# Kernel tuning notes

Hardware: AMD Instinct MI355X
Metric: run time of the kernel (lower is better)

The kernel has to match this reference:

```python
import jax, jax.numpy as jnp
import numpy as np

B, S, D, H = 4, 2048, 1024, 16
DK = D // H


def setup_inputs() -> dict:
    key = jax.random.key(0)
    ks = jax.random.split(key, 11)
    inp = {
        'query': jax.random.normal(ks[0], (B, S, D), jnp.float32),
        'key': jax.random.normal(ks[1], (B, S, D), jnp.float32),
        'value': jax.random.normal(ks[2], (B, S, D), jnp.float32),
        'mask': jnp.tril(jnp.ones((1, 1, S, S), dtype=bool)),  # causal
    }
    sc = 1.0 / np.sqrt(D)
    inp['w_q'] = jax.random.normal(ks[3], (D, D), jnp.float32) * sc
    inp['b_q'] = jnp.zeros((D,), jnp.float32)
    inp['w_k'] = jax.random.normal(ks[4], (D, D), jnp.float32) * sc
    inp['b_k'] = jnp.zeros((D,), jnp.float32)
    inp['w_v'] = jax.random.normal(ks[5], (D, D), jnp.float32) * sc
    inp['b_v'] = jnp.zeros((D,), jnp.float32)
    inp['w_o'] = jax.random.normal(ks[6], (D, D), jnp.float32) * sc
    inp['b_o'] = jnp.zeros((D,), jnp.float32)
    return inp


def _split_heads(x):
    # Faithful to source: view(B, S, d_k, H) then permute(0,3,1,2)
    b, s, _ = x.shape
    return x.reshape(b, s, DK, H).transpose(0, 3, 1, 2)  # (B, H, S, DK)


def _concat_heads(x):
    # permute(0,2,1,3) -> reshape(B, S, d_k*H)
    b, h, s, dk = x.shape
    return x.transpose(0, 2, 1, 3).reshape(b, s, dk * h)


def reference(query, key, value, mask, w_q, b_q, w_k, b_k, w_v, b_v, w_o, b_o):
    q = query @ w_q.T + b_q
    k = key @ w_k.T + b_k
    v = value @ w_v.T + b_v
    q, k, v = _split_heads(q), _split_heads(k), _split_heads(v)
    scale = 1.0 / jnp.sqrt(jnp.asarray(DK, q.dtype))
    scores = jnp.einsum('bhqd,bhkd->bhqk', q, k) * scale
    scores = jnp.where(mask, scores, -jnp.inf)
    attn = jax.nn.softmax(scores, axis=-1)  # dropout p=0 -> identity
    out = jnp.einsum('bhqk,bhkd->bhqd', attn, v)
    return _concat_heads(out) @ w_o.T + b_o
```

## Files before the change

### kernel.cpp

```cpp
#include <hip/hip_runtime.h>

#define BB 4
#define SS 2048
#define DD 1024
#define HH 16
#define DK 64
#define MM (BB * SS)

typedef __bf16 bf16x8 __attribute__((ext_vector_type(8)));
typedef float f32x4 __attribute__((ext_vector_type(4)));
typedef unsigned short us8 __attribute__((ext_vector_type(8)));
typedef unsigned short us4 __attribute__((ext_vector_type(4)));

#define MFMA_BF16(a, b, c) __builtin_amdgcn_mfma_f32_16x16x32_bf16((a), (b), (c), 0, 0, 0)

__device__ __forceinline__ unsigned short f2bf(float f) {
  return __builtin_bit_cast(unsigned short, (__bf16)f);
}

__device__ __forceinline__ bf16x8 ld_frag(const unsigned short* p) {
  return __builtin_bit_cast(bf16x8, *(const us8*)p);
}

__device__ __forceinline__ void gl_lds16(const unsigned short* g, unsigned short* l) {
  __builtin_amdgcn_global_load_lds((const __attribute__((address_space(1))) void*)g,
                                   (__attribute__((address_space(3))) void*)l, 16, 0, 0);
}

__global__ void cvt_weights(const float* __restrict__ w0, const float* __restrict__ w1,
                            const float* __restrict__ w2, const float* __restrict__ w3,
                            unsigned short* __restrict__ dst) {
  const float* src = (blockIdx.y == 0) ? w0 : (blockIdx.y == 1) ? w1 : (blockIdx.y == 2) ? w2 : w3;
  unsigned short* d = dst + (size_t)blockIdx.y * (DD * DD);
  int idx = (blockIdx.x * 256 + threadIdx.x) * 4;
  float4 v = *(const float4*)(src + idx);
  us4 o;
  o[0] = f2bf(v.x); o[1] = f2bf(v.y); o[2] = f2bf(v.z); o[3] = f2bf(v.w);
  *(us4*)(d + idx) = o;
}

__global__ __launch_bounds__(256, 4) void qkv_gemm(
    const float* __restrict__ xq, const float* __restrict__ xk, const float* __restrict__ xv,
    const unsigned short* __restrict__ wb,
    const float* __restrict__ bq, const float* __restrict__ bk, const float* __restrict__ bv,
    unsigned short* __restrict__ qh, unsigned short* __restrict__ kh,
    unsigned short* __restrict__ vt) {
  const int mode = blockIdx.z;
  const float* x = (mode == 0) ? xq : (mode == 1) ? xk : xv;
  const unsigned short* w = wb + (size_t)mode * (DD * DD);
  const float* bias = (mode == 0) ? bq : (mode == 1) ? bk : bv;

  const int m0 = blockIdx.x * 128;
  const int h0 = blockIdx.y * 2;

  __shared__ unsigned short smem[17408];
  unsigned short* sA = smem;
  unsigned short* sB = smem + 8192;

  const int tid = threadIdx.x;
  const int lane = tid & 63;
  const int wave = tid >> 6;
  const int wm = wave & 1, wn = wave >> 1;
  const int quad = lane >> 4, l16 = lane & 15;

  f32x4 acc[4][4];
#pragma unroll
  for (int i = 0; i < 4; i++)
#pragma unroll
    for (int j = 0; j < 4; j++) acc[i][j] = f32x4{0.f, 0.f, 0.f, 0.f};

  const int arow = tid >> 1, ahalf = tid & 1;
  const float* ag = x + (size_t)(m0 + arow) * DD + ahalf * 32;
  unsigned short* adst = sA + ahalf * 4096 + arow * 32;

  for (int k0 = 0; k0 < DD; k0 += 64) {
    __syncthreads();
#pragma unroll
    for (int j = 0; j < 4; j++) {
      int cid = tid + j * 256;
      int half = cid >> 9;
      int rr = (cid & 511) >> 2;
      int c8 = (cid & 3) << 3;
      int n = ((rr & 63) << 4) + h0 + (rr >> 6);
      gl_lds16(w + (size_t)n * DD + k0 + half * 32 + c8,
               sB + half * 4096 + rr * 32 + c8);
    }
    {
      const float* a = ag + k0;
      float4 v0 = *(const float4*)(a + 0);
      float4 v1 = *(const float4*)(a + 4);
      float4 v2 = *(const float4*)(a + 8);
      float4 v3 = *(const float4*)(a + 12);
      float4 v4 = *(const float4*)(a + 16);
      float4 v5 = *(const float4*)(a + 20);
      float4 v6 = *(const float4*)(a + 24);
      float4 v7 = *(const float4*)(a + 28);
      us8 o0, o1, o2, o3;
      o0[0] = f2bf(v0.x); o0[1] = f2bf(v0.y); o0[2] = f2bf(v0.z); o0[3] = f2bf(v0.w);
      o0[4] = f2bf(v1.x); o0[5] = f2bf(v1.y); o0[6] = f2bf(v1.z); o0[7] = f2bf(v1.w);
      o1[0] = f2bf(v2.x); o1[1] = f2bf(v2.y); o1[2] = f2bf(v2.z); o1[3] = f2bf(v2.w);
      o1[4] = f2bf(v3.x); o1[5] = f2bf(v3.y); o1[6] = f2bf(v3.z); o1[7] = f2bf(v3.w);
      o2[0] = f2bf(v4.x); o2[1] = f2bf(v4.y); o2[2] = f2bf(v4.z); o2[3] = f2bf(v4.w);
      o2[4] = f2bf(v5.x); o2[5] = f2bf(v5.y); o2[6] = f2bf(v5.z); o2[7] = f2bf(v5.w);
      o3[0] = f2bf(v6.x); o3[1] = f2bf(v6.y); o3[2] = f2bf(v6.z); o3[3] = f2bf(v6.w);
      o3[4] = f2bf(v7.x); o3[5] = f2bf(v7.y); o3[6] = f2bf(v7.z); o3[7] = f2bf(v7.w);
      *(us8*)(adst + 0) = o0;
      *(us8*)(adst + 8) = o1;
      *(us8*)(adst + 16) = o2;
      *(us8*)(adst + 24) = o3;
    }
    __syncthreads();
#pragma unroll
    for (int kk = 0; kk < 2; kk++) {
      bf16x8 af[4];
#pragma unroll
      for (int mi = 0; mi < 4; mi++)
        af[mi] = ld_frag(sA + kk * 4096 + (wm * 64 + mi * 16 + l16) * 32 + quad * 8);
#pragma unroll
      for (int ni = 0; ni < 4; ni++) {
        bf16x8 bfr = ld_frag(sB + kk * 4096 + (wn * 64 + ni * 16 + l16) * 32 + quad * 8);
#pragma unroll
        for (int mi = 0; mi < 4; mi++) acc[mi][ni] = MFMA_BF16(af[mi], bfr, acc[mi][ni]);
      }
    }
  }

  if (mode < 2) {
    unsigned short* outp = (mode == 0) ? qh : kh;
#pragma unroll
    for (int mi = 0; mi < 4; mi++) {
#pragma unroll
      for (int ni = 0; ni < 4; ni++) {
        int c = wn * 64 + ni * 16 + l16;
        int h = h0 + (c >> 6), dk = c & 63;
        float bvv = bias[(dk << 4) + h];
        int mg0 = m0 + wm * 64 + mi * 16 + quad * 4;
#pragma unroll
        for (int r = 0; r < 4; r++) {
          int mg = mg0 + r;
          int bb = mg >> 11, s = mg & 2047;
          size_t dst = ((size_t)((bb << 4) + h) * SS + s) * DK + dk;
          outp[dst] = f2bf(acc[mi][ni][r] + bvv);
        }
      }
    }
  } else {
    __syncthreads();
#pragma unroll
    for (int mi = 0; mi < 4; mi++) {
#pragma unroll
      for (int ni = 0; ni < 4; ni++) {
        int c = wn * 64 + ni * 16 + l16;
        int h = h0 + (c >> 6), dk = c & 63;
        float bvv = bias[(dk << 4) + h];
        int ml0 = wm * 64 + mi * 16 + quad * 4;
#pragma unroll
        for (int r = 0; r < 4; r++)
          smem[c * 136 + ml0 + r] = f2bf(acc[mi][ni][r] + bvv);
      }
    }
    __syncthreads();
    int bb = m0 >> 11;
    int sbase = m0 & 2047;
#pragma unroll
    for (int i = 0; i < 8; i++) {
      int idx = tid + i * 256;
      int c = idx >> 4, mc = (idx & 15) << 3;
      int h = h0 + (c >> 6), dk = c & 63;
      size_t dst = ((size_t)((bb << 4) + h) * DK + dk) * SS + sbase + mc;
      *(us8*)(vt + dst) = *(const us8*)(smem + c * 136 + mc);
    }
  }
}

__global__ __launch_bounds__(256, 2) void attn(
    const unsigned short* __restrict__ qh, const unsigned short* __restrict__ kh,
    const unsigned short* __restrict__ vt, unsigned short* __restrict__ outc) {
  const int bh = blockIdx.x;
  const int by = blockIdx.y;
  const int b = bh >> 4, h = bh & 15;
  const unsigned short* Qp = qh + (size_t)bh * SS * DK;
  const unsigned short* Kp = kh + (size_t)bh * SS * DK;
  const unsigned short* Vp = vt + (size_t)bh * DK * SS;

  __shared__ unsigned short sK[128 * 72];
  __shared__ unsigned short sV[64 * 136];

  const int tid = threadIdx.x;
  const int lane = tid & 63;
  const int wave = tid >> 6;
  const int quad = lane >> 4, l16 = lane & 15;
  const int wq0 = wave * 32;

  const float sl = 0.125f * 1.44269504088896f;

  for (int pass = 0; pass < 2; pass++) {
    const int qt = pass ? (15 - by) : by;
    const int q0 = qt * 128;

    bf16x8 aq[2][2];
#pragma unroll
    for (int mi = 0; mi < 2; mi++)
#pragma unroll
      for (int kk = 0; kk < 2; kk++)
        aq[mi][kk] = ld_frag(Qp + (size_t)(q0 + wq0 + mi * 16 + l16) * DK + kk * 32 + quad * 8);

    f32x4 o_acc[2][4];
    float mrowL[2], lrowL[2];
#pragma unroll
    for (int mi = 0; mi < 2; mi++) {
#pragma unroll
      for (int ni = 0; ni < 4; ni++) o_acc[mi][ni] = f32x4{0.f, 0.f, 0.f, 0.f};
      mrowL[mi] = -1e30f;
      lrowL[mi] = 0.f;
    }

    for (int kt = 0; kt <= qt; kt++) {
      const int k0 = kt * 128;
      const bool diag = (kt == qt);
      __syncthreads();
#pragma unroll
      for (int i = 0; i < 4; i++) {
        int idx = tid + i * 256;
        int row = idx >> 3, c8 = (idx & 7) << 3;
        *(us8*)(sK + row * 72 + c8) = *(const us8*)(Kp + (size_t)(k0 + row) * DK + c8);
      }
#pragma unroll
      for (int i = 0; i < 4; i++) {
        int idx = tid + i * 256;
        int row = idx >> 4, cc = (idx & 15) << 3;
        *(us8*)(sV + row * 136 + cc) = *(const us8*)(Vp + (size_t)row * SS + k0 + cc);
      }
      __syncthreads();

      f32x4 sc[2][8];
#pragma unroll
      for (int mi = 0; mi < 2; mi++)
#pragma unroll
        for (int kti = 0; kti < 8; kti++) sc[mi][kti] = f32x4{0.f, 0.f, 0.f, 0.f};
#pragma unroll
      for (int kti = 0; kti < 8; kti++) {
#pragma unroll
        for (int kk = 0; kk < 2; kk++) {
          bf16x8 ak = ld_frag(sK + (kti * 16 + l16) * 72 + kk * 32 + quad * 8);
#pragma unroll
          for (int mi = 0; mi < 2; mi++) sc[mi][kti] = MFMA_BF16(ak, aq[mi][kk], sc[mi][kti]);
        }
      }

      if (diag) {
#pragma unroll
        for (int mi = 0; mi < 2; mi++) {
          int ql = wq0 + mi * 16 + l16;
#pragma unroll
          for (int kti = 0; kti < 8; kti++)
#pragma unroll
            for (int r = 0; r < 4; r++) {
              int kl = kti * 16 + quad * 4 + r;
              float v = sc[mi][kti][r] * sl;
              sc[mi][kti][r] = (kl > ql) ? -1e30f : v;
            }
        }
      } else {
#pragma unroll
        for (int mi = 0; mi < 2; mi++)
#pragma unroll
          for (int kti = 0; kti < 8; kti++)
#pragma unroll
            for (int r = 0; r < 4; r++) sc[mi][kti][r] *= sl;
      }

      float alphaL[2];
#pragma unroll
      for (int mi = 0; mi < 2; mi++) {
        f32x4 vm = sc[mi][0];
#pragma unroll
        for (int kti = 1; kti < 8; kti++)
#pragma unroll
          for (int r = 0; r < 4; r++) vm[r] = fmaxf(vm[r], sc[mi][kti][r]);
        float mx = fmaxf(fmaxf(vm[0], vm[1]), fmaxf(vm[2], vm[3]));
        mx = fmaxf(mx, __shfl_xor(mx, 16, 64));
        mx = fmaxf(mx, __shfl_xor(mx, 32, 64));
        float mnew = fmaxf(mrowL[mi], mx);
        alphaL[mi] = exp2f(mrowL[mi] - mnew);
        mrowL[mi] = mnew;
      }

#pragma unroll
      for (int mi = 0; mi < 2; mi++) {
#pragma unroll
        for (int r = 0; r < 4; r++) {
          float a = __shfl(alphaL[mi], quad * 4 + r, 64);
#pragma unroll
          for (int ni = 0; ni < 4; ni++) o_acc[mi][ni][r] *= a;
        }
        us4 pk[8];
        f32x4 vs = f32x4{0.f, 0.f, 0.f, 0.f};
#pragma unroll
        for (int kti = 0; kti < 8; kti++) {
#pragma unroll
          for (int r = 0; r < 4; r++) {
            float p = exp2f(sc[mi][kti][r] - mrowL[mi]);
            vs[r] += p;
            pk[kti][r] = f2bf(p);
          }
        }
        float ls = (vs[0] + vs[1]) + (vs[2] + vs[3]);
        ls += __shfl_xor(ls, 16, 64);
        ls += __shfl_xor(ls, 32, 64);
        lrowL[mi] = lrowL[mi] * alphaL[mi] + ls;

#pragma unroll
        for (int c = 0; c < 4; c++) {
          bf16x8 ap = __builtin_bit_cast(
              bf16x8, __builtin_shufflevector(pk[2 * c], pk[2 * c + 1], 0, 1, 2, 3, 4, 5, 6, 7));
#pragma unroll
          for (int ni = 0; ni < 4; ni++) {
            const unsigned short* vb = sV + (ni * 16 + l16) * 136 + c * 32 + quad * 4;
            us4 lo = *(const us4*)vb;
            us4 hi = *(const us4*)(vb + 16);
            bf16x8 bfr = __builtin_bit_cast(
                bf16x8, __builtin_shufflevector(lo, hi, 0, 1, 2, 3, 4, 5, 6, 7));
            o_acc[mi][ni] = MFMA_BF16(ap, bfr, o_acc[mi][ni]);
          }
        }
      }
    }

#pragma unroll
    for (int mi = 0; mi < 2; mi++) {
#pragma unroll
      for (int r = 0; r < 4; r++) {
        float lr = __shfl(lrowL[mi], quad * 4 + r, 64);
        float inv = 1.0f / lr;
        int qg = q0 + wq0 + mi * 16 + quad * 4 + r;
        size_t rowbase = ((size_t)(b * SS + qg)) * DD + h * DK;
#pragma unroll
        for (int ni = 0; ni < 4; ni++) {
          int dk = ni * 16 + l16;
          outc[rowbase + dk] = f2bf(o_acc[mi][ni][r] * inv);
        }
      }
    }
    __syncthreads();
  }
}

__global__ __launch_bounds__(256, 4) void out_proj(
    const unsigned short* __restrict__ ac, const unsigned short* __restrict__ wo,
    const float* __restrict__ bias, float* __restrict__ out) {
  const int m0 = blockIdx.x * 128;
  const int n0 = blockIdx.y * 128;
  __shared__ unsigned short sA[8192];
  __shared__ unsigned short sB[8192];

  const int tid = threadIdx.x;
  const int lane = tid & 63;
  const int wave = tid >> 6;
  const int wm = wave & 1, wn = wave >> 1;
  const int quad = lane >> 4, l16 = lane & 15;

  f32x4 acc[4][4];
#pragma unroll
  for (int i = 0; i < 4; i++)
#pragma unroll
    for (int j = 0; j < 4; j++) acc[i][j] = f32x4{0.f, 0.f, 0.f, 0.f};

  for (int k0 = 0; k0 < DD; k0 += 64) {
    __syncthreads();
#pragma unroll
    for (int j = 0; j < 4; j++) {
      int cid = tid + j * 256;
      int half = cid >> 9;
      int rr = (cid & 511) >> 2;
      int c8 = (cid & 3) << 3;
      gl_lds16(ac + (size_t)(m0 + rr) * DD + k0 + half * 32 + c8,
               sA + half * 4096 + rr * 32 + c8);
    }
#pragma unroll
    for (int j = 0; j < 4; j++) {
      int cid = tid + j * 256;
      int half = cid >> 9;
      int rr = (cid & 511) >> 2;
      int c8 = (cid & 3) << 3;
      gl_lds16(wo + (size_t)(n0 + rr) * DD + k0 + half * 32 + c8,
               sB + half * 4096 + rr * 32 + c8);
    }
    __syncthreads();
#pragma unroll
    for (int kk = 0; kk < 2; kk++) {
      bf16x8 af[4];
#pragma unroll
      for (int mi = 0; mi < 4; mi++)
        af[mi] = ld_frag(sA + kk * 4096 + (wm * 64 + mi * 16 + l16) * 32 + quad * 8);
#pragma unroll
      for (int ni = 0; ni < 4; ni++) {
        bf16x8 bfr = ld_frag(sB + kk * 4096 + (wn * 64 + ni * 16 + l16) * 32 + quad * 8);
#pragma unroll
        for (int mi = 0; mi < 4; mi++) acc[mi][ni] = MFMA_BF16(af[mi], bfr, acc[mi][ni]);
      }
    }
  }

#pragma unroll
  for (int mi = 0; mi < 4; mi++) {
#pragma unroll
    for (int ni = 0; ni < 4; ni++) {
      int n = n0 + wn * 64 + ni * 16 + l16;
      float bvv = bias[n];
      int mg0 = m0 + wm * 64 + mi * 16 + quad * 4;
#pragma unroll
      for (int r = 0; r < 4; r++) out[(size_t)(mg0 + r) * DD + n] = acc[mi][ni][r] + bvv;
    }
  }
}

extern "C" void kernel_launch(void* const* d_in, const int* in_sizes, int n_in,
                              void* d_out, int out_size, void* d_ws, size_t ws_size,
                              hipStream_t stream) {
  const float* q_in = (const float*)d_in[0];
  const float* k_in = (const float*)d_in[1];
  const float* v_in = (const float*)d_in[2];
  const float* w_q = (const float*)d_in[4];
  const float* b_q = (const float*)d_in[5];
  const float* w_k = (const float*)d_in[6];
  const float* b_k = (const float*)d_in[7];
  const float* w_v = (const float*)d_in[8];
  const float* b_v = (const float*)d_in[9];
  const float* w_o = (const float*)d_in[10];
  const float* b_o = (const float*)d_in[11];
  float* out = (float*)d_out;

  unsigned short* ws = (unsigned short*)d_ws;
  unsigned short* wb = ws;
  unsigned short* qh = ws + (size_t)4 * 1024 * 1024;
  unsigned short* kh = ws + (size_t)12 * 1024 * 1024;
  unsigned short* vt = ws + (size_t)20 * 1024 * 1024;
  unsigned short* outc = ws + (size_t)28 * 1024 * 1024;

  const size_t WSZ = (size_t)DD * DD;

  cvt_weights<<<dim3(1024, 4), 256, 0, stream>>>(w_q, w_k, w_v, w_o, wb);
  qkv_gemm<<<dim3(64, 8, 3), 256, 0, stream>>>(q_in, k_in, v_in, wb, b_q, b_k, b_v, qh, kh, vt);
  attn<<<dim3(64, 8), 256, 0, stream>>>(qh, kh, vt, outc);
  out_proj<<<dim3(64, 8), 256, 0, stream>>>(outc, wb + 3 * WSZ, b_o, out);
}
```

Before: 374.6 us.

## Prefetch next K-tile into registers and swizzle A tile in LDS for QKV GEMM

The QKV projection GEMM now loads the next K-step's fp32 activations and bf16 weights into registers while MFMAs run on the current tile. It replaces the direct global-to-LDS weight loads with register-staged stores, and hoists the per-iteration address arithmetic out of the loop. The A tile in LDS gets an XOR swizzle on 8-element chunks to reduce bank conflicts on fragment reads. The extra live registers force launch bounds to drop from 4 to 3 blocks per SM, trading occupancy for overlap.

```diff
diff --git a/kernel.cpp b/kernel.cpp
--- a/kernel.cpp
+++ b/kernel.cpp
@@ -39,7 +39,7 @@
   *(us4*)(d + idx) = o;
 }
 
-__global__ __launch_bounds__(256, 4) void qkv_gemm(
+__global__ __launch_bounds__(256, 3) void qkv_gemm(
     const float* __restrict__ xq, const float* __restrict__ xk, const float* __restrict__ xv,
     const unsigned short* __restrict__ wb,
     const float* __restrict__ bq, const float* __restrict__ bk, const float* __restrict__ bv,
@@ -71,51 +71,57 @@
 
   const int arow = tid >> 1, ahalf = tid & 1;
   const float* ag = x + (size_t)(m0 + arow) * DD + ahalf * 32;
-  unsigned short* adst = sA + ahalf * 4096 + arow * 32;
+  unsigned short* arow_base = sA + ahalf * 4096 + arow * 32;
+  const int asw = (arow >> 1) & 3;
+
+  const unsigned short* bsrc[4];
+  unsigned short* bdst[4];
+#pragma unroll
+  for (int j = 0; j < 4; j++) {
+    int cid = tid + j * 256;
+    int half = cid >> 9, rr = (cid & 511) >> 2, c8 = (cid & 3) << 3;
+    int n = ((rr & 63) << 4) + h0 + (rr >> 6);
+    bsrc[j] = w + (size_t)n * DD + half * 32 + c8;
+    bdst[j] = sB + half * 4096 + rr * 32 + c8;
+  }
+
+  float4 va[8];
+  us8 vbr[4];
+#pragma unroll
+  for (int i = 0; i < 8; i++) va[i] = *(const float4*)(ag + 0 + i * 4);
+#pragma unroll
+  for (int j = 0; j < 4; j++) vbr[j] = *(const us8*)(bsrc[j] + 0);
 
   for (int k0 = 0; k0 < DD; k0 += 64) {
     __syncthreads();
 #pragma unroll
-    for (int j = 0; j < 4; j++) {
-      int cid = tid + j * 256;
-      int half = cid >> 9;
-      int rr = (cid & 511) >> 2;
-      int c8 = (cid & 3) << 3;
-      int n = ((rr & 63) << 4) + h0 + (rr >> 6);
-      gl_lds16(w + (size_t)n * DD + k0 + half * 32 + c8,
-               sB + half * 4096 + rr * 32 + c8);
-    }
-    {
-      const float* a = ag + k0;
-      float4 v0 = *(const float4*)(a + 0);
-      float4 v1 = *(const float4*)(a + 4);
-      float4 v2 = *(const float4*)(a + 8);
-      float4 v3 = *(const float4*)(a + 12);
-      float4 v4 = *(const float4*)(a + 16);
-      float4 v5 = *(const float4*)(a + 20);
-      float4 v6 = *(const float4*)(a + 24);
-      float4 v7 = *(const float4*)(a + 28);
-      us8 o0, o1, o2, o3;
-      o0[0] = f2bf(v0.x); o0[1] = f2bf(v0.y); o0[2] = f2bf(v0.z); o0[3] = f2bf(v0.w);
-      o0[4] = f2bf(v1.x); o0[5] = f2bf(v1.y); o0[6] = f2bf(v1.z); o0[7] = f2bf(v1.w);
-      o1[0] = f2bf(v2.x); o1[1] = f2bf(v2.y); o1[2] = f2bf(v2.z); o1[3] = f2bf(v2.w);
-      o1[4] = f2bf(v3.x); o1[5] = f2bf(v3.y); o1[6] = f2bf(v3.z); o1[7] = f2bf(v3.w);
-      o2[0] = f2bf(v4.x); o2[1] = f2bf(v4.y); o2[2] = f2bf(v4.z); o2[3] = f2bf(v4.w);
-      o2[4] = f2bf(v5.x); o2[5] = f2bf(v5.y); o2[6] = f2bf(v5.z); o2[7] = f2bf(v5.w);
-      o3[0] = f2bf(v6.x); o3[1] = f2bf(v6.y); o3[2] = f2bf(v6.z); o3[3] = f2bf(v6.w);
-      o3[4] = f2bf(v7.x); o3[5] = f2bf(v7.y); o3[6] = f2bf(v7.z); o3[7] = f2bf(v7.w);
-      *(us8*)(adst + 0) = o0;
-      *(us8*)(adst + 8) = o1;
-      *(us8*)(adst + 16) = o2;
-      *(us8*)(adst + 24) = o3;
-    }
-    __syncthreads();
+    for (int c = 0; c < 4; c++) {
+      us8 o;
+      o[0] = f2bf(va[2 * c].x); o[1] = f2bf(va[2 * c].y);
+      o[2] = f2bf(va[2 * c].z); o[3] = f2bf(va[2 * c].w);
+      o[4] = f2bf(va[2 * c + 1].x); o[5] = f2bf(va[2 * c + 1].y);
+      o[6] = f2bf(va[2 * c + 1].z); o[7] = f2bf(va[2 * c + 1].w);
+      *(us8*)(arow_base + ((c ^ asw) << 3)) = o;
+    }
+#pragma unroll
+    for (int j = 0; j < 4; j++) *(us8*)(bdst[j]) = vbr[j];
+    __syncthreads();
+
+    if (k0 + 64 < DD) {
+#pragma unroll
+      for (int i = 0; i < 8; i++) va[i] = *(const float4*)(ag + k0 + 64 + i * 4);
+#pragma unroll
+      for (int j = 0; j < 4; j++) vbr[j] = *(const us8*)(bsrc[j] + k0 + 64);
+    }
+
 #pragma unroll
     for (int kk = 0; kk < 2; kk++) {
       bf16x8 af[4];
 #pragma unroll
-      for (int mi = 0; mi < 4; mi++)
-        af[mi] = ld_frag(sA + kk * 4096 + (wm * 64 + mi * 16 + l16) * 32 + quad * 8);
+      for (int mi = 0; mi < 4; mi++) {
+        int row = wm * 64 + mi * 16 + l16;
+        af[mi] = ld_frag(sA + kk * 4096 + row * 32 + ((quad ^ ((row >> 1) & 3)) << 3));
+      }
 #pragma unroll
       for (int ni = 0; ni < 4; ni++) {
         bf16x8 bfr = ld_frag(sB + kk * 4096 + (wn * 64 + ni * 16 + l16) * 32 + quad * 8);
```

After: 370.8 us. Within noise of the previous version (-1.0%).
